# Optimization experiments

Hardware: AMD Instinct MI355X
Metric: run time of the kernel (lower is better)

## Reference

```python
import jax, jax.numpy as jnp
import numpy as np

N_NODES = 50000
N_EDGES = 800000
N_GRAPHS = 1024
N_PAIRS = 16384
N_CL = 16
IN_CH = 64
EMB = 128
HID = 256
OUT = 1


def _xavier(key, shape):
    fan_in, fan_out = shape[-2], shape[-1]
    lim = (6.0 / (fan_in + fan_out)) ** 0.5
    return jax.random.uniform(key, shape, jnp.float32, -lim, lim)


def setup_inputs() -> dict:
    key = jax.random.key(0)
    ks = jax.random.split(key, 12)
    x = jax.random.normal(ks[0], (N_NODES, IN_CH), jnp.float32)
    edge_index = jax.random.randint(ks[1], (2, N_EDGES), 0, N_NODES)
    batch = jnp.sort(jax.random.randint(ks[2], (N_NODES,), 0, N_GRAPHS))
    drug_drug_batch = jax.random.randint(ks[3], (2, N_PAIRS), 0, N_GRAPHS)
    edge_cell_lines = jax.random.randint(ks[4], (N_PAIRS,), 0, N_CL)
    conv1_w = _xavier(ks[5], (IN_CH, EMB))
    conv2_w = _xavier(ks[6], (EMB, EMB))
    reg_w1 = _xavier(ks[7], (N_CL, 2 * EMB, HID))
    reg_w2 = _xavier(ks[8], (N_CL, HID, OUT))
    return dict(
        x=x,
        conv1_w=conv1_w, conv1_b=jnp.zeros((EMB,), jnp.float32),
        conv2_w=conv2_w, conv2_b=jnp.zeros((EMB,), jnp.float32),
        reg_w1=reg_w1, reg_b1=jnp.zeros((N_CL, HID), jnp.float32),
        reg_w2=reg_w2, reg_b2=jnp.zeros((N_CL, OUT), jnp.float32),
        edge_index=edge_index, batch=batch,
        drug_drug_batch=drug_drug_batch, edge_cell_lines=edge_cell_lines,
    )


def _forward(x, conv1_w, conv1_b, conv2_w, conv2_b,
             reg_w1, reg_b1, reg_w2, reg_b2,
             edge_index, batch, drug_drug_batch, edge_cell_lines):
    n = x.shape[0]
    # GCN normalization with self-loops (PyG GCNConv default)
    loop = jnp.arange(n)
    row = jnp.concatenate([edge_index[0], loop])  # source
    col = jnp.concatenate([edge_index[1], loop])  # target
    deg = jax.ops.segment_sum(jnp.ones(row.shape[0], x.dtype), col, num_segments=n)
    dinv = jnp.where(deg > 0, jax.lax.rsqrt(deg), 0.0)
    norm = dinv[row] * dinv[col]  # [E+N]

    def gcn(h, W, b):
        hw = h @ W
        agg = jax.ops.segment_sum(norm[:, None] * hw[row], col, num_segments=n)
        return agg + b

    h = jax.nn.relu(gcn(x, conv1_w, conv1_b))
    h = jax.nn.relu(gcn(h, conv2_w, conv2_b))

    # scatter-mean pooling over graphs
    gsum = jax.ops.segment_sum(h, batch, num_segments=N_GRAPHS)
    cnt = jax.ops.segment_sum(jnp.ones(n, h.dtype), batch, num_segments=N_GRAPHS)
    graph_embeds = gsum / jnp.maximum(cnt, 1.0)[:, None]

    # np.digitize(ddb, unique(ddb)+1); with contiguous ids 0..G-1 this is identity,
    # expressed faithfully via searchsorted against bins = arange(G)+1
    bins = jnp.arange(N_GRAPHS) + 1
    q = jnp.searchsorted(bins, drug_drug_batch, side='right')
    pair = jnp.concatenate([graph_embeds[q[0]], graph_embeds[q[1]]], axis=1)  # [P, 2*EMB]

    # per-cell-line Linear-ReLU-Linear, computed for all lines then selected
    hcl = jax.nn.relu(jnp.einsum('pe,ceh->pch', pair, reg_w1) + reg_b1[None])  # [P,C,H]
    ocl = jnp.einsum('pch,cho->pco', hcl, reg_w2) + reg_b2[None]               # [P,C,O]
    preds = jnp.take_along_axis(ocl, edge_cell_lines[:, None, None], axis=1)[:, 0, :]
    return preds


def reference(x, conv1_w, conv1_b, conv2_w, conv2_b,
              reg_w1, reg_b1, reg_w2, reg_b2,
              edge_index, batch, drug_drug_batch, edge_cell_lines):
    return _forward(x, conv1_w, conv1_b, conv2_w, conv2_b,
                    reg_w1, reg_b1, reg_w2, reg_b2,
                    edge_index, batch, drug_drug_batch, edge_cell_lines)
```

## Files before the change

kernel.cpp:

```cpp
#include <hip/hip_runtime.h>
#include <hip/hip_fp16.h>

#define NN 50000
#define NE 800000
#define NG 1024
#define NP 16384
#define NCL 16
#define INCH 64
#define EMB 128
#define HID 256

#define NB 391
#define NCHUNK 400
#define EPB 2000

#define CDIV(a,b) (((a)+(b)-1)/(b))

typedef _Float16 f16x8 __attribute__((ext_vector_type(8)));
typedef float    f32x4 __attribute__((ext_vector_type(4)));
typedef unsigned short ushort_t;

template<int NW>
__device__ __forceinline__ int block_excl_scan(int v, int t, int* incl_out) {
    int lane = t & 63, w = t >> 6;
    int s = v;
#pragma unroll
    for (int d = 1; d < 64; d <<= 1) {
        int u = __shfl_up(s, d, 64);
        if (lane >= d) s += u;
    }
    __shared__ int wsum[NW];
    if (lane == 63) wsum[w] = s;
    __syncthreads();
    int add = 0;
    for (int k = 0; k < w; ++k) add += wsum[k];
    *incl_out = s + add;
    return s + add - v;
}

__global__ __launch_bounds__(256) void k_prep(const float* __restrict__ c1w,
                                              const float* __restrict__ c2w,
                                              const float* __restrict__ rw1,
                                              const int* __restrict__ batch,
                                              __half* __restrict__ w1t,
                                              __half* __restrict__ w2t,
                                              __half* __restrict__ Whl,
                                              float* __restrict__ inv) {
    int bid = blockIdx.x, t = threadIdx.x;
    if (bid < 512) {
        int i = bid * 256 + t;
        int ch = i & 15, tg = (i >> 4) & 255, z = i >> 12;
        int c = z >> 1, part = z & 1;
        f16x8 hi, lo;
#pragma unroll
        for (int j = 0; j < 8; ++j) {
            float v = rw1[(size_t)c * 65536 + (size_t)(part * 128 + ch * 8 + j) * 256 + tg];
            _Float16 h = (_Float16)v;
            hi[j] = h;
            lo[j] = (_Float16)(v - (float)h);
        }
        size_t base = ((size_t)z * 256 + tg) * 16 + ch;
        ((f16x8*)Whl)[base] = hi;
        ((f16x8*)Whl)[(size_t)32 * 256 * 16 + base] = lo;
    } else if (bid < 544) {
        int i = (bid - 512) * 256 + t;
        int k = i >> 7, n = i & 127;
        w1t[n * INCH + k] = __float2half(c1w[i]);
    } else if (bid < 608) {
        int i = (bid - 544) * 256 + t;
        int k = i >> 7, n = i & 127;
        w2t[n * EMB + k] = __float2half(c2w[i]);
    } else {
        int g = (bid - 608) * 256 + t;
        int lo_ = 0, hi_ = NN;
        while (lo_ < hi_) { int m = (lo_ + hi_) >> 1; if (batch[m] < g) lo_ = m + 1; else hi_ = m; }
        int s = lo_;
        lo_ = 0; hi_ = NN;
        while (lo_ < hi_) { int m = (lo_ + hi_) >> 1; if (batch[m] < g + 1) lo_ = m + 1; else hi_ = m; }
        float c = (float)(lo_ - s);
        inv[g] = 1.f / fmaxf(c, 1.f);
    }
}

__global__ __launch_bounds__(256) void k_cnt(const int* __restrict__ cols,
                                             int* __restrict__ cnt) {
    __shared__ int hist[NB];
    int ch = blockIdx.x, t = threadIdx.x;
    for (int b = t; b < NB; b += 256) hist[b] = 0;
    __syncthreads();
    for (int e = ch * EPB + t; e < (ch + 1) * EPB; e += 256)
        atomicAdd(&hist[cols[e] >> 7], 1);
    __syncthreads();
    for (int b = t; b < NB; b += 256) cnt[b * NCHUNK + ch] = hist[b];
}

__global__ __launch_bounds__(512) void k_bscan(int* __restrict__ cnt,
                                               int* __restrict__ btot) {
    int b = blockIdx.x, t = threadIdx.x;
    int v = (t < NCHUNK) ? cnt[b * NCHUNK + t] : 0;
    int incl;
    int excl = block_excl_scan<8>(v, t, &incl);
    if (t < NCHUNK) cnt[b * NCHUNK + t] = excl;
    if (t == NCHUNK - 1) btot[b] = incl;
}

__global__ __launch_bounds__(256) void k_part(const int* __restrict__ rows,
                                              const int* __restrict__ cols,
                                              const int* __restrict__ cnt,
                                              const int* __restrict__ btot,
                                              int* __restrict__ bbase_out,
                                              int* __restrict__ ebuf) {
    __shared__ int bb[NB + 1];
    __shared__ int cur[NB];
    __shared__ int S0s;
    int ch = blockIdx.x, t = threadIdx.x;
    int incl;
    int v0 = btot[t];
    int e0 = block_excl_scan<4>(v0, t, &incl);
    bb[t] = e0;
    if (t == 255) S0s = incl;
    __syncthreads();
    int t2 = t + 256;
    int v1 = (t2 < NB) ? btot[t2] : 0;
    int e1 = block_excl_scan<4>(v1, t, &incl);
    if (t2 <= NB) bb[t2] = e1 + S0s;
    __syncthreads();
    for (int b = t; b < NB; b += 256) cur[b] = bb[b] + cnt[b * NCHUNK + ch];
    if (ch == 0)
        for (int i = t; i <= NB; i += 256) bbase_out[i] = bb[i];
    __syncthreads();
    for (int e = ch * EPB + t; e < (ch + 1) * EPB; e += 256) {
        int c = cols[e], r = rows[e];
        int pos = atomicAdd(&cur[c >> 7], 1);
        ebuf[pos] = (r << 7) | (c & 127);
    }
}

__global__ __launch_bounds__(256) void k_bsort(const int* __restrict__ ebuf,
                                               const int* __restrict__ bbase,
                                               const float* __restrict__ x,
                                               int* __restrict__ off,
                                               float* __restrict__ dinv,
                                               ushort_t* __restrict__ srows,
                                               __half* __restrict__ xs) {
    __shared__ int   ldeg[128];
    __shared__ int   lcur[128];
    __shared__ float ldinv[128];
    int b = blockIdx.x, t = threadIdx.x;
    int n0 = b << 7;
    int nloc = min(128, NN - n0);
    int beg = bbase[b], end = bbase[b + 1];
    if (t < 128) ldeg[t] = 0;
    __syncthreads();
    for (int i = beg + t; i < end; i += 256)
        atomicAdd(&ldeg[ebuf[i] & 127], 1);
    __syncthreads();
    int v = (t < nloc) ? ldeg[t] : 0;
    int incl;
    int excl = block_excl_scan<4>(v, t, &incl);
    if (t < nloc) {
        off[n0 + t]  = beg + excl + v;
        float d = rsqrtf((float)(v + 1));
        dinv[n0 + t] = d;
        ldinv[t] = d;
        lcur[t] = beg + excl;
    }
    __syncthreads();
    for (int i = beg + t; i < end; i += 256) {
        int e = ebuf[i];
        int pos = atomicAdd(&lcur[e & 127], 1);
        srows[pos] = (ushort_t)(e >> 7);
    }
    const float4* Xx = (const float4*)x;
#pragma unroll
    for (int i = 0; i < 8; ++i) {
        int f4 = t + i * 256;
        int rloc = f4 >> 4, kq = f4 & 15;
        if (rloc < nloc) {
            float d = ldinv[rloc];
            float4 vv = Xx[(size_t)(n0 + rloc) * 16 + kq];
            __half2 h[2];
            h[0] = __floats2half2_rn(d * vv.x, d * vv.y);
            h[1] = __floats2half2_rn(d * vv.z, d * vv.w);
            ((float2*)xs)[(size_t)(n0 + rloc) * 16 + kq] = *(float2*)h;
        }
    }
}

template<int FEAT, bool ZB>
__global__ __launch_bounds__(256) void k_gath_h(const int* __restrict__ off,
                                                const ushort_t* __restrict__ srows,
                                                const float* __restrict__ dinv,
                                                const __half* __restrict__ SRC,
                                                __half* __restrict__ DST,
                                                float* __restrict__ zbuf) {
    if (ZB) {
        if (blockIdx.x < 512) zbuf[(blockIdx.x << 8) + threadIdx.x] = 0.f;
    }
    constexpr int NC = FEAT / 8;
    constexpr int PL = NC / 8;
    int node = blockIdx.x * 4 + (threadIdx.x >> 6);
    int lane = threadIdx.x & 63;
    int slot = lane >> 3, q = lane & 7;
    if (node >= NN) return;
    int beg = node ? off[node - 1] : 0;
    int end = off[node];
    float di = dinv[node];
    const float4* S4 = (const float4*)SRC;

    float acc[PL][8];
#pragma unroll
    for (int i = 0; i < PL; ++i)
#pragma unroll
        for (int j = 0; j < 8; ++j) acc[i][j] = 0.f;

    if (slot == 0) {
#pragma unroll
        for (int i = 0; i < PL; ++i) {
            float4 raw = S4[node * NC + i * 8 + q];
            const __half2* h = (const __half2*)&raw;
#pragma unroll
            for (int j = 0; j < 4; ++j) {
                float2 f = __half22float2(h[j]);
                acc[i][2 * j + 0] = f.x;
                acc[i][2 * j + 1] = f.y;
            }
        }
    }
    for (int e = beg + slot; e < end; e += 8) {
        int r = srows[e];
#pragma unroll
        for (int i = 0; i < PL; ++i) {
            float4 raw = S4[r * NC + i * 8 + q];
            const __half2* h = (const __half2*)&raw;
#pragma unroll
            for (int j = 0; j < 4; ++j) {
                float2 f = __half22float2(h[j]);
                acc[i][2 * j + 0] += f.x;
                acc[i][2 * j + 1] += f.y;
            }
        }
    }
#pragma unroll
    for (int d = 8; d < 64; d <<= 1)
#pragma unroll
        for (int i = 0; i < PL; ++i)
#pragma unroll
            for (int j = 0; j < 8; ++j)
                acc[i][j] += __shfl_xor(acc[i][j], d, 64);

    if (lane < 8) {
        float4* D4 = (float4*)DST;
#pragma unroll
        for (int i = 0; i < PL; ++i) {
            float4 pk;
            __half2* hp = (__half2*)&pk;
            hp[0] = __floats2half2_rn(di * acc[i][0], di * acc[i][1]);
            hp[1] = __floats2half2_rn(di * acc[i][2], di * acc[i][3]);
            hp[2] = __floats2half2_rn(di * acc[i][4], di * acc[i][5]);
            hp[3] = __floats2half2_rn(di * acc[i][6], di * acc[i][7]);
            D4[node * NC + i * 8 + lane] = pk;
        }
    }
}

template<int K, bool RS, bool POOL>
__global__ __launch_bounds__(256) void gemm_mf(const __half* __restrict__ X,
                                               const __half* __restrict__ WT,
                                               const float* __restrict__ bias,
                                               const float* __restrict__ rs,
                                               const int* __restrict__ batch,
                                               float* __restrict__ Y, int M) {
    constexpr int KP = K + 8;
    __shared__ __half Xs[64 * KP];
    __shared__ __half Ws[128 * KP];
    __shared__ int sb[64];
    const int t = threadIdx.x;
    const int row0 = blockIdx.x * 64;

    const float4* X8 = (const float4*)X;
#pragma unroll
    for (int i = t; i < 64 * (K / 8); i += 256) {
        int r = i / (K / 8), ch = i % (K / 8);
        float4 v = make_float4(0.f, 0.f, 0.f, 0.f);
        if (row0 + r < M) v = X8[(size_t)(row0 + r) * (K / 8) + ch];
        *(float4*)&Xs[r * KP + ch * 8] = v;
    }
    const float4* W8 = (const float4*)WT;
#pragma unroll
    for (int i = t; i < 128 * (K / 8); i += 256) {
        int n = i / (K / 8), ch = i % (K / 8);
        *(float4*)&Ws[n * KP + ch * 8] = W8[i];
    }
    if (POOL) {
        if (t < 64) sb[t] = (row0 + t < M) ? batch[row0 + t] : -1;
    }
    __syncthreads();

    const int w  = t >> 6;
    const int l  = t & 63;
    const int lm = l & 15, lg = l >> 4;

    f32x4 acc[8];
#pragma unroll
    for (int c = 0; c < 8; ++c) acc[c] = (f32x4){0.f, 0.f, 0.f, 0.f};

#pragma unroll
    for (int kk = 0; kk < K / 32; ++kk) {
        f16x8 a = *(const f16x8*)&Xs[(16 * w + lm) * KP + kk * 32 + lg * 8];
#pragma unroll
        for (int c = 0; c < 8; ++c) {
            f16x8 bf = *(const f16x8*)&Ws[(16 * c + lm) * KP + kk * 32 + lg * 8];
            acc[c] = __builtin_amdgcn_mfma_f32_16x16x32_f16(a, bf, acc[c], 0, 0, 0);
        }
    }

    float bcol[8];
#pragma unroll
    for (int c = 0; c < 8; ++c) bcol[c] = bias[16 * c + lm];

    if (POOL) {
#pragma unroll
        for (int c = 0; c < 8; ++c) {
            int rung = -1;
            float run = 0.f;
#pragma unroll
            for (int j = 0; j < 4; ++j) {
                int rr = 16 * w + 4 * lg + j;
                int g = (row0 + rr < M) ? sb[rr] : -1;
                if (g != rung) {
                    if (rung >= 0) atomicAdd(&Y[rung * 128 + 16 * c + lm], run);
                    run = 0.f;
                    rung = g;
                }
                if (g >= 0) run += fmaxf(acc[c][j] + bcol[c], 0.f);
            }
            if (rung >= 0) atomicAdd(&Y[rung * 128 + 16 * c + lm], run);
        }
        return;
    }

    __half* Yh = (__half*)Y;
#pragma unroll
    for (int j = 0; j < 4; ++j) {
        int r = row0 + 16 * w + 4 * lg + j;
        if (r < M) {
            float d = RS ? rs[r] : 1.f;
#pragma unroll
            for (int c = 0; c < 8; ++c) {
                float v = d * fmaxf(acc[c][j] + bcol[c], 0.f);
                Yh[(size_t)r * 128 + 16 * c + lm] = __float2half(v);
            }
        }
    }
}

__global__ __launch_bounds__(256) void gemm_bat(const float* __restrict__ gsum,
                                                const float* __restrict__ inv,
                                                const __half* __restrict__ Whl,
                                                float* __restrict__ Aarr,
                                                float* __restrict__ Barr) {
    constexpr int KP = 128 + 8;
    __shared__ __half Xs[64 * KP];
    __shared__ __half Ws[128 * KP];
    const int t = threadIdx.x;
    const int row0 = blockIdx.x * 64;
    const int y = blockIdx.y, z = blockIdx.z;

    const float4* G4 = (const float4*)gsum;
#pragma unroll
    for (int i = t; i < 64 * 16; i += 256) {
        int r = i >> 4, ch = i & 15;
        int g = row0 + r;
        float iv = inv[g];
        float4 a = G4[g * 32 + ch * 2];
        float4 b4 = G4[g * 32 + ch * 2 + 1];
        float4 pk;
        __half2* hp = (__half2*)&pk;
        hp[0] = __floats2half2_rn(iv * a.x, iv * a.y);
        hp[1] = __floats2half2_rn(iv * a.z, iv * a.w);
        hp[2] = __floats2half2_rn(iv * b4.x, iv * b4.y);
        hp[3] = __floats2half2_rn(iv * b4.z, iv * b4.w);
        *(float4*)&Xs[r * KP + ch * 8] = pk;
    }

    const int w  = t >> 6;
    const int l  = t & 63;
    const int lm = l & 15, lg = l >> 4;

    f32x4 acc[8];
#pragma unroll
    for (int c = 0; c < 8; ++c) acc[c] = (f32x4){0.f, 0.f, 0.f, 0.f};

    const float4* W8 = (const float4*)Whl;
#pragma unroll
    for (int pass = 0; pass < 2; ++pass) {
        __syncthreads();
        size_t wbase = ((size_t)pass * 32 + z) * 256 * 16;
#pragma unroll
        for (int i = t; i < 128 * 16; i += 256) {
            int n = i >> 4, ch = i & 15;
            *(float4*)&Ws[n * KP + ch * 8] = W8[wbase + (size_t)(y * 128 + n) * 16 + ch];
        }
        __syncthreads();
#pragma unroll
        for (int kk = 0; kk < 4; ++kk) {
            f16x8 a = *(const f16x8*)&Xs[(16 * w + lm) * KP + kk * 32 + lg * 8];
#pragma unroll
            for (int c = 0; c < 8; ++c) {
                f16x8 bf = *(const f16x8*)&Ws[(16 * c + lm) * KP + kk * 32 + lg * 8];
                acc[c] = __builtin_amdgcn_mfma_f32_16x16x32_f16(a, bf, acc[c], 0, 0, 0);
            }
        }
    }

    float* Obase = (z & 1) ? Barr : Aarr;
#pragma unroll
    for (int j = 0; j < 4; ++j) {
        int g = row0 + 16 * w + 4 * lg + j;
        size_t rb = ((size_t)(z >> 1) * NG + g) * HID + y * 128;
#pragma unroll
        for (int c = 0; c < 8; ++c)
            Obase[rb + 16 * c + lm] = acc[c][j];
    }
}

__global__ __launch_bounds__(256) void k_pair(const float* __restrict__ Aarr,
                                              const float* __restrict__ Barr,
                                              const int* __restrict__ ddb,
                                              const int* __restrict__ ecl,
                                              const float* __restrict__ B1,
                                              const float* __restrict__ W2,
                                              const float* __restrict__ B2,
                                              float* __restrict__ out) {
    int p = blockIdx.x * 4 + (threadIdx.x >> 6);
    int lane = threadIdx.x & 63;
    int c = ecl[p];
    int a = ddb[p];
    int b = ddb[NP + p];
    const float4* rA = (const float4*)&Aarr[((size_t)c * NG + a) * HID];
    const float4* rB = (const float4*)&Barr[((size_t)c * NG + b) * HID];
    const float4* b1 = (const float4*)&B1[c * HID];
    const float4* w2 = (const float4*)&W2[c * HID];
    float4 va = rA[lane], vb = rB[lane], v1 = b1[lane], v2 = w2[lane];
    float hx = va.x + vb.x + v1.x;
    float hy = va.y + vb.y + v1.y;
    float hz = va.z + vb.z + v1.z;
    float hw = va.w + vb.w + v1.w;
    float s = 0.f;
    s = fmaf(hx > 0.f ? hx : 0.f, v2.x, s);
    s = fmaf(hy > 0.f ? hy : 0.f, v2.y, s);
    s = fmaf(hz > 0.f ? hz : 0.f, v2.z, s);
    s = fmaf(hw > 0.f ? hw : 0.f, v2.w, s);
    for (int o = 32; o; o >>= 1) s += __shfl_down(s, o, 64);
    if (lane == 0) out[p] = s + B2[c];
}

extern "C" void kernel_launch(void* const* d_in, const int* in_sizes, int n_in,
                              void* d_out, int out_size, void* d_ws, size_t ws_size,
                              hipStream_t stream) {
    const float* x    = (const float*)d_in[0];
    const float* c1w  = (const float*)d_in[1];
    const float* c1b  = (const float*)d_in[2];
    const float* c2w  = (const float*)d_in[3];
    const float* c2b  = (const float*)d_in[4];
    const float* rw1  = (const float*)d_in[5];
    const float* rb1  = (const float*)d_in[6];
    const float* rw2  = (const float*)d_in[7];
    const float* rb2  = (const float*)d_in[8];
    const int*   eidx = (const int*)d_in[9];
    const int*   batch= (const int*)d_in[10];
    const int*   ddb  = (const int*)d_in[11];
    const int*   ecl  = (const int*)d_in[12];
    float* out = (float*)d_out;

    int*   off   = (int*)d_ws;
    int*   srows = off + 50048;
    float* dinv  = (float*)(srows + NE);
    float* bufA  = dinv + 50048;
    float* bufB  = bufA + NN * EMB;

    int*      ebuf  = (int*)bufA;
    int*      cnt   = (int*)(bufB + 1700000);
    int*      btot  = cnt + NB * NCHUNK;
    int*      bbase = btot + 512;
    __half*   xs    = (__half*)bufB;
    __half*   aggXh = (__half*)bufA;
    __half*   H1h   = (__half*)bufB;
    __half*   aggHh = (__half*)bufA;
    float*    gsum  = bufA + 4500000;
    __half*   w1t   = (__half*)(bufA + 4700000);
    __half*   w2t   = (__half*)(bufA + 4710000);
    float*    inv   = bufA + 4730000;
    __half*   Whl   = (__half*)(bufB + 4300000);
    float*    Aarr  = bufA;
    float*    Barr  = bufB;
    ushort_t* srowsU = (ushort_t*)srows;

    const int* erow = eidx;
    const int* ecol = eidx + NE;

    k_prep<<<612, 256, 0, stream>>>(c1w, c2w, rw1, batch, w1t, w2t, Whl, inv);

    k_cnt  <<<NCHUNK, 256, 0, stream>>>(ecol, cnt);
    k_bscan<<<NB,     512, 0, stream>>>(cnt, btot);
    k_part <<<NCHUNK, 256, 0, stream>>>(erow, ecol, cnt, btot, bbase, ebuf);
    k_bsort<<<NB,     256, 0, stream>>>(ebuf, bbase, x, off, dinv, srowsU, xs);

    k_gath_h<INCH,true><<<CDIV(NN,4),256,0,stream>>>(off, srowsU, dinv, xs, aggXh, gsum);
    gemm_mf<INCH,true,false><<<CDIV(NN,64),256,0,stream>>>(aggXh, w1t, c1b, dinv, nullptr, (float*)H1h, NN);

    k_gath_h<EMB,false><<<CDIV(NN,4),256,0,stream>>>(off, srowsU, dinv, H1h, aggHh, nullptr);
    gemm_mf<EMB,false,true><<<CDIV(NN,64),256,0,stream>>>(aggHh, w2t, c2b, nullptr, batch, gsum, NN);

    dim3 bgrid(NG/64, 2, 2*NCL);
    gemm_bat<<<bgrid,256,0,stream>>>(gsum, inv, Whl, Aarr, Barr);
    k_pair<<<NP/4,256,0,stream>>>(Aarr, Barr, ddb, ecl, rb1, rw2, rb2, out);
}
```

Before: 162.5 us.

## Fuse neighbor gather into MFMA GEMM and merge edge histogram into prep kernel

The sparse neighbor aggregation is now done inside the GEMM kernel: each block gathers its 64 destination rows straight into shared memory and then runs the MFMA matmul, so the half-precision aggregated intermediate no longer goes through global memory. The edge-count histogram kernel is folded into the weight-prep launch, removing one launch. In exchange, gather parallelism drops from one node per wave across 12.5k blocks to 16 nodes per wave serially across about 782 blocks, which may cut latency hiding for the irregular loads.

```diff
diff --git a/kernel.cpp b/kernel.cpp
--- a/kernel.cpp
+++ b/kernel.cpp
@@ -38,17 +38,28 @@
     return s + add - v;
 }
 
-__global__ __launch_bounds__(256) void k_prep(const float* __restrict__ c1w,
-                                              const float* __restrict__ c2w,
-                                              const float* __restrict__ rw1,
-                                              const int* __restrict__ batch,
-                                              __half* __restrict__ w1t,
-                                              __half* __restrict__ w2t,
-                                              __half* __restrict__ Whl,
-                                              float* __restrict__ inv) {
+__global__ __launch_bounds__(256) void k_prep0(const int* __restrict__ cols,
+                                               const float* __restrict__ c1w,
+                                               const float* __restrict__ c2w,
+                                               const float* __restrict__ rw1,
+                                               const int* __restrict__ batch,
+                                               int* __restrict__ cnt,
+                                               __half* __restrict__ w1t,
+                                               __half* __restrict__ w2t,
+                                               __half* __restrict__ Whl,
+                                               float* __restrict__ inv) {
+    __shared__ int hist[NB];
     int bid = blockIdx.x, t = threadIdx.x;
-    if (bid < 512) {
-        int i = bid * 256 + t;
+    if (bid < 400) {
+        int ch = bid;
+        for (int b = t; b < NB; b += 256) hist[b] = 0;
+        __syncthreads();
+        for (int e = ch * EPB + t; e < (ch + 1) * EPB; e += 256)
+            atomicAdd(&hist[cols[e] >> 7], 1);
+        __syncthreads();
+        for (int b = t; b < NB; b += 256) cnt[b * NCHUNK + ch] = hist[b];
+    } else if (bid < 912) {
+        int i = (bid - 400) * 256 + t;
         int ch = i & 15, tg = (i >> 4) & 255, z = i >> 12;
         int c = z >> 1, part = z & 1;
         f16x8 hi, lo;
@@ -62,16 +73,16 @@
         size_t base = ((size_t)z * 256 + tg) * 16 + ch;
         ((f16x8*)Whl)[base] = hi;
         ((f16x8*)Whl)[(size_t)32 * 256 * 16 + base] = lo;
-    } else if (bid < 544) {
-        int i = (bid - 512) * 256 + t;
+    } else if (bid < 944) {
+        int i = (bid - 912) * 256 + t;
         int k = i >> 7, n = i & 127;
         w1t[n * INCH + k] = __float2half(c1w[i]);
-    } else if (bid < 608) {
-        int i = (bid - 544) * 256 + t;
+    } else if (bid < 1008) {
+        int i = (bid - 944) * 256 + t;
         int k = i >> 7, n = i & 127;
         w2t[n * EMB + k] = __float2half(c2w[i]);
     } else {
-        int g = (bid - 608) * 256 + t;
+        int g = (bid - 1008) * 256 + t;
         int lo_ = 0, hi_ = NN;
         while (lo_ < hi_) { int m = (lo_ + hi_) >> 1; if (batch[m] < g) lo_ = m + 1; else hi_ = m; }
         int s = lo_;
@@ -80,18 +91,6 @@
         float c = (float)(lo_ - s);
         inv[g] = 1.f / fmaxf(c, 1.f);
     }
-}
-
-__global__ __launch_bounds__(256) void k_cnt(const int* __restrict__ cols,
-                                             int* __restrict__ cnt) {
-    __shared__ int hist[NB];
-    int ch = blockIdx.x, t = threadIdx.x;
-    for (int b = t; b < NB; b += 256) hist[b] = 0;
-    __syncthreads();
-    for (int e = ch * EPB + t; e < (ch + 1) * EPB; e += 256)
-        atomicAdd(&hist[cols[e] >> 7], 1);
-    __syncthreads();
-    for (int b = t; b < NB; b += 256) cnt[b * NCHUNK + ch] = hist[b];
 }
 
 __global__ __launch_bounds__(512) void k_bscan(int* __restrict__ cnt,
@@ -187,123 +186,109 @@
     }
 }
 
-template<int FEAT, bool ZB>
-__global__ __launch_bounds__(256) void k_gath_h(const int* __restrict__ off,
-                                                const ushort_t* __restrict__ srows,
-                                                const float* __restrict__ dinv,
-                                                const __half* __restrict__ SRC,
-                                                __half* __restrict__ DST,
-                                                float* __restrict__ zbuf) {
-    if (ZB) {
-        if (blockIdx.x < 512) zbuf[(blockIdx.x << 8) + threadIdx.x] = 0.f;
-    }
-    constexpr int NC = FEAT / 8;
+template<int K, bool RS, bool POOL, bool ZB>
+__global__ __launch_bounds__(256) void k_gg(const int* __restrict__ off,
+                                            const ushort_t* __restrict__ srows,
+                                            const float* __restrict__ dinv,
+                                            const __half* __restrict__ SRC,
+                                            const __half* __restrict__ WT,
+                                            const float* __restrict__ bias,
+                                            const float* __restrict__ rs,
+                                            const int* __restrict__ batch,
+                                            float* __restrict__ Y,
+                                            float* __restrict__ zbuf,
+                                            int M) {
+    constexpr int KP = K + 8;
+    constexpr int NC = K / 8;
     constexpr int PL = NC / 8;
-    int node = blockIdx.x * 4 + (threadIdx.x >> 6);
-    int lane = threadIdx.x & 63;
-    int slot = lane >> 3, q = lane & 7;
-    if (node >= NN) return;
-    int beg = node ? off[node - 1] : 0;
-    int end = off[node];
-    float di = dinv[node];
-    const float4* S4 = (const float4*)SRC;
-
-    float acc[PL][8];
-#pragma unroll
-    for (int i = 0; i < PL; ++i)
-#pragma unroll
-        for (int j = 0; j < 8; ++j) acc[i][j] = 0.f;
-
-    if (slot == 0) {
-#pragma unroll
-        for (int i = 0; i < PL; ++i) {
-            float4 raw = S4[node * NC + i * 8 + q];
-            const __half2* h = (const __half2*)&raw;
-#pragma unroll
-            for (int j = 0; j < 4; ++j) {
-                float2 f = __half22float2(h[j]);
-                acc[i][2 * j + 0] = f.x;
-                acc[i][2 * j + 1] = f.y;
-            }
-        }
-    }
-    for (int e = beg + slot; e < end; e += 8) {
-        int r = srows[e];
-#pragma unroll
-        for (int i = 0; i < PL; ++i) {
-            float4 raw = S4[r * NC + i * 8 + q];
-            const __half2* h = (const __half2*)&raw;
-#pragma unroll
-            for (int j = 0; j < 4; ++j) {
-                float2 f = __half22float2(h[j]);
-                acc[i][2 * j + 0] += f.x;
-                acc[i][2 * j + 1] += f.y;
-            }
-        }
-    }
-#pragma unroll
-    for (int d = 8; d < 64; d <<= 1)
-#pragma unroll
-        for (int i = 0; i < PL; ++i)
-#pragma unroll
-            for (int j = 0; j < 8; ++j)
-                acc[i][j] += __shfl_xor(acc[i][j], d, 64);
-
-    if (lane < 8) {
-        float4* D4 = (float4*)DST;
-#pragma unroll
-        for (int i = 0; i < PL; ++i) {
-            float4 pk;
-            __half2* hp = (__half2*)&pk;
-            hp[0] = __floats2half2_rn(di * acc[i][0], di * acc[i][1]);
-            hp[1] = __floats2half2_rn(di * acc[i][2], di * acc[i][3]);
-            hp[2] = __floats2half2_rn(di * acc[i][4], di * acc[i][5]);
-            hp[3] = __floats2half2_rn(di * acc[i][6], di * acc[i][7]);
-            D4[node * NC + i * 8 + lane] = pk;
-        }
-    }
-}
-
-template<int K, bool RS, bool POOL>
-__global__ __launch_bounds__(256) void gemm_mf(const __half* __restrict__ X,
-                                               const __half* __restrict__ WT,
-                                               const float* __restrict__ bias,
-                                               const float* __restrict__ rs,
-                                               const int* __restrict__ batch,
-                                               float* __restrict__ Y, int M) {
-    constexpr int KP = K + 8;
     __shared__ __half Xs[64 * KP];
     __shared__ __half Ws[128 * KP];
     __shared__ int sb[64];
     const int t = threadIdx.x;
     const int row0 = blockIdx.x * 64;
 
-    const float4* X8 = (const float4*)X;
-#pragma unroll
-    for (int i = t; i < 64 * (K / 8); i += 256) {
-        int r = i / (K / 8), ch = i % (K / 8);
-        float4 v = make_float4(0.f, 0.f, 0.f, 0.f);
-        if (row0 + r < M) v = X8[(size_t)(row0 + r) * (K / 8) + ch];
-        *(float4*)&Xs[r * KP + ch * 8] = v;
-    }
+    if (ZB) {
+        if (blockIdx.x < 512) zbuf[(blockIdx.x << 8) + t] = 0.f;
+    }
+
     const float4* W8 = (const float4*)WT;
 #pragma unroll
-    for (int i = t; i < 128 * (K / 8); i += 256) {
-        int n = i / (K / 8), ch = i % (K / 8);
+    for (int i = t; i < 128 * NC; i += 256) {
+        int n = i / NC, ch = i % NC;
         *(float4*)&Ws[n * KP + ch * 8] = W8[i];
     }
-    if (POOL) {
-        if (t < 64) sb[t] = (row0 + t < M) ? batch[row0 + t] : -1;
-    }
-    __syncthreads();
-
-    const int w  = t >> 6;
-    const int l  = t & 63;
+    if (POOL && t < 64) sb[t] = (row0 + t < M) ? batch[row0 + t] : -1;
+
+    const int w = t >> 6, l = t & 63;
+    const int slot = l >> 3, q = l & 7;
+    const float4* S4 = (const float4*)SRC;
+    for (int i = 0; i < 16; ++i) {
+        int rloc = 16 * w + i;
+        int node = row0 + rloc;
+        float acc[PL][8];
+#pragma unroll
+        for (int p = 0; p < PL; ++p)
+#pragma unroll
+            for (int j = 0; j < 8; ++j) acc[p][j] = 0.f;
+        float di = 0.f;
+        if (node < M) {
+            int beg = node ? off[node - 1] : 0;
+            int end = off[node];
+            di = dinv[node];
+            if (slot == 0) {
+#pragma unroll
+                for (int p = 0; p < PL; ++p) {
+                    float4 raw = S4[(size_t)node * NC + p * 8 + q];
+                    const __half2* h = (const __half2*)&raw;
+#pragma unroll
+                    for (int j = 0; j < 4; ++j) {
+                        float2 f = __half22float2(h[j]);
+                        acc[p][2 * j + 0] = f.x;
+                        acc[p][2 * j + 1] = f.y;
+                    }
+                }
+            }
+            for (int e = beg + slot; e < end; e += 8) {
+                int r = srows[e];
+#pragma unroll
+                for (int p = 0; p < PL; ++p) {
+                    float4 raw = S4[(size_t)r * NC + p * 8 + q];
+                    const __half2* h = (const __half2*)&raw;
+#pragma unroll
+                    for (int j = 0; j < 4; ++j) {
+                        float2 f = __half22float2(h[j]);
+                        acc[p][2 * j + 0] += f.x;
+                        acc[p][2 * j + 1] += f.y;
+                    }
+                }
+            }
+        }
+#pragma unroll
+        for (int d = 8; d < 64; d <<= 1)
+#pragma unroll
+            for (int p = 0; p < PL; ++p)
+#pragma unroll
+                for (int j = 0; j < 8; ++j)
+                    acc[p][j] += __shfl_xor(acc[p][j], d, 64);
+        if (l < 8) {
+#pragma unroll
+            for (int p = 0; p < PL; ++p) {
+                float4 pk;
+                __half2* hp = (__half2*)&pk;
+                hp[0] = __floats2half2_rn(di * acc[p][0], di * acc[p][1]);
+                hp[1] = __floats2half2_rn(di * acc[p][2], di * acc[p][3]);
+                hp[2] = __floats2half2_rn(di * acc[p][4], di * acc[p][5]);
+                hp[3] = __floats2half2_rn(di * acc[p][6], di * acc[p][7]);
+                *(float4*)&Xs[rloc * KP + (p * 8 + l) * 8] = pk;
+            }
+        }
+    }
+    __syncthreads();
+
     const int lm = l & 15, lg = l >> 4;
-
-    f32x4 acc[8];
-#pragma unroll
-    for (int c = 0; c < 8; ++c) acc[c] = (f32x4){0.f, 0.f, 0.f, 0.f};
+    f32x4 macc[8];
+#pragma unroll
+    for (int c = 0; c < 8; ++c) macc[c] = (f32x4){0.f, 0.f, 0.f, 0.f};
 
 #pragma unroll
     for (int kk = 0; kk < K / 32; ++kk) {
@@ -311,7 +296,7 @@
 #pragma unroll
         for (int c = 0; c < 8; ++c) {
             f16x8 bf = *(const f16x8*)&Ws[(16 * c + lm) * KP + kk * 32 + lg * 8];
-            acc[c] = __builtin_amdgcn_mfma_f32_16x16x32_f16(a, bf, acc[c], 0, 0, 0);
+            macc[c] = __builtin_amdgcn_mfma_f32_16x16x32_f16(a, bf, macc[c], 0, 0, 0);
         }
     }
 
@@ -333,7 +318,7 @@
                     run = 0.f;
                     rung = g;
                 }
-                if (g >= 0) run += fmaxf(acc[c][j] + bcol[c], 0.f);
+                if (g >= 0) run += fmaxf(macc[c][j] + bcol[c], 0.f);
             }
             if (rung >= 0) atomicAdd(&Y[rung * 128 + 16 * c + lm], run);
         }
@@ -348,7 +333,7 @@
             float d = RS ? rs[r] : 1.f;
 #pragma unroll
             for (int c = 0; c < 8; ++c) {
-                float v = d * fmaxf(acc[c][j] + bcol[c], 0.f);
+                float v = d * fmaxf(macc[c][j] + bcol[c], 0.f);
                 Yh[(size_t)r * 128 + 16 * c + lm] = __float2half(v);
             }
         }
@@ -485,9 +470,7 @@
     int*      btot  = cnt + NB * NCHUNK;
     int*      bbase = btot + 512;
     __half*   xs    = (__half*)bufB;
-    __half*   aggXh = (__half*)bufA;
-    __half*   H1h   = (__half*)bufB;
-    __half*   aggHh = (__half*)bufA;
+    __half*   H1h   = (__half*)bufA;
     float*    gsum  = bufA + 4500000;
     __half*   w1t   = (__half*)(bufA + 4700000);
     __half*   w2t   = (__half*)(bufA + 4710000);
@@ -500,18 +483,18 @@
     const int* erow = eidx;
     const int* ecol = eidx + NE;
 
-    k_prep<<<612, 256, 0, stream>>>(c1w, c2w, rw1, batch, w1t, w2t, Whl, inv);
-
-    k_cnt  <<<NCHUNK, 256, 0, stream>>>(ecol, cnt);
-    k_bscan<<<NB,     512, 0, stream>>>(cnt, btot);
+    k_prep0<<<1012, 256, 0, stream>>>(ecol, c1w, c2w, rw1, batch,
+                                      cnt, w1t, w2t, Whl, inv);
+
+    k_bscan<<<NB,  512, 0, stream>>>(cnt, btot);
     k_part <<<NCHUNK, 256, 0, stream>>>(erow, ecol, cnt, btot, bbase, ebuf);
-    k_bsort<<<NB,     256, 0, stream>>>(ebuf, bbase, x, off, dinv, srowsU, xs);
-
-    k_gath_h<INCH,true><<<CDIV(NN,4),256,0,stream>>>(off, srowsU, dinv, xs, aggXh, gsum);
-    gemm_mf<INCH,true,false><<<CDIV(NN,64),256,0,stream>>>(aggXh, w1t, c1b, dinv, nullptr, (float*)H1h, NN);
-
-    k_gath_h<EMB,false><<<CDIV(NN,4),256,0,stream>>>(off, srowsU, dinv, H1h, aggHh, nullptr);
-    gemm_mf<EMB,false,true><<<CDIV(NN,64),256,0,stream>>>(aggHh, w2t, c2b, nullptr, batch, gsum, NN);
+    k_bsort<<<NB,  256, 0, stream>>>(ebuf, bbase, x, off, dinv, srowsU, xs);
+
+    k_gg<INCH,true,false,true><<<CDIV(NN,64),256,0,stream>>>(
+        off, srowsU, dinv, xs, w1t, c1b, dinv, nullptr, (float*)H1h, gsum, NN);
+
+    k_gg<EMB,false,true,false><<<CDIV(NN,64),256,0,stream>>>(
+        off, srowsU, dinv, H1h, w2t, c2b, nullptr, batch, gsum, nullptr, NN);
 
     dim3 bgrid(NG/64, 2, 2*NCL);
     gemm_bat<<<bgrid,256,0,stream>>>(gsum, inv, Whl, Aarr, Barr);
```

New measurement: 209.9 us. 29.2% more time.
